# Performance work log

Hardware: AMD Instinct MI355X
Metric: run time of the kernel (lower is better)

Reference implementation:

```python
import jax, jax.numpy as jnp
import numpy as np

N = 50000      # nodes
E = 800000     # edges (before self-loops)
IN = 128       # in_channels
HID = 16       # hidden_channels
HEADS = 8
OUT = 16       # out_channels
NEG_SLOPE = 0.2
BN_EPS = 1e-5
LN_EPS = 1e-5


def setup_inputs() -> dict:
    key = jax.random.key(0)
    ks = jax.random.split(key, 16)
    s = 0.05
    inp = {
        "x": jax.random.normal(ks[0], (N, IN), jnp.float32),
        "edge_index": jax.random.randint(ks[1], (2, E), 0, N, jnp.int64),
        # conv1 (in=IN, out=HID, heads=HEADS, concat=True)
        "Wl1": jax.random.normal(ks[2], (HEADS * HID, IN), jnp.float32) * s,
        "bl1": jnp.zeros((HEADS * HID,), jnp.float32),
        "Wr1": jax.random.normal(ks[3], (HEADS * HID, IN), jnp.float32) * s,
        "br1": jnp.zeros((HEADS * HID,), jnp.float32),
        "att1": jax.random.normal(ks[4], (HEADS, HID), jnp.float32) * s,
        "bias1": jnp.zeros((HEADS * HID,), jnp.float32),
        # batchnorm (eval mode, running stats)
        "bn_w": jnp.ones((HEADS * HID,), jnp.float32),
        "bn_b": jnp.zeros((HEADS * HID,), jnp.float32),
        "bn_rm": jnp.zeros((HEADS * HID,), jnp.float32),
        "bn_rv": jnp.ones((HEADS * HID,), jnp.float32),
        # conv2 (in=HEADS*HID, out=OUT, heads=HEADS, concat=False)
        "Wl2": jax.random.normal(ks[5], (HEADS * OUT, HEADS * HID), jnp.float32) * s,
        "bl2": jnp.zeros((HEADS * OUT,), jnp.float32),
        "Wr2": jax.random.normal(ks[6], (HEADS * OUT, HEADS * HID), jnp.float32) * s,
        "br2": jnp.zeros((HEADS * OUT,), jnp.float32),
        "att2": jax.random.normal(ks[7], (HEADS, OUT), jnp.float32) * s,
        "bias2": jnp.zeros((OUT,), jnp.float32),
        # skip + layernorm
        "Wskip": jax.random.normal(ks[8], (OUT, IN), jnp.float32) * s,
        "ln_w": jnp.ones((OUT,), jnp.float32),
        "ln_b": jnp.zeros((OUT,), jnp.float32),
    }
    return inp


def _gatv2(x, src, dst, Wl, bl, Wr, br, att, bias, heads, ch, concat):
    """PyG GATv2Conv (share_weights=False), eval mode (no dropout)."""
    n = x.shape[0]
    xl = (x @ Wl.T + bl).reshape(n, heads, ch)   # source transform
    xr = (x @ Wr.T + br).reshape(n, heads, ch)   # target transform
    # edge-wise attention score
    e = jax.nn.leaky_relu(xl[src] + xr[dst], NEG_SLOPE)          # [E',H,C]
    score = jnp.einsum('ehc,hc->eh', e, att)                      # [E',H]
    # segment softmax over incoming edges per destination node
    smax = jax.ops.segment_max(score, dst, num_segments=n)
    ex = jnp.exp(score - smax[dst])
    denom = jax.ops.segment_sum(ex, dst, num_segments=n)
    alpha = ex / denom[dst]                                       # [E',H]
    out = jax.ops.segment_sum(alpha[:, :, None] * xl[src], dst, num_segments=n)
    if concat:
        out = out.reshape(n, heads * ch)
    else:
        out = out.mean(axis=1)
    return out + bias


def reference(x, edge_index, Wl1, bl1, Wr1, br1, att1, bias1,
              bn_w, bn_b, bn_rm, bn_rv,
              Wl2, bl2, Wr2, br2, att2, bias2,
              Wskip, ln_w, ln_b):
    n = x.shape[0]
    loops = jnp.arange(n, dtype=edge_index.dtype)
    src = jnp.concatenate([edge_index[0], loops])
    dst = jnp.concatenate([edge_index[1], loops])

    x_res = x @ Wskip.T                                            # [N,OUT]

    h = _gatv2(x, src, dst, Wl1, bl1, Wr1, br1, att1, bias1, HEADS, HID, True)
    # BatchNorm1d in eval mode
    h = (h - bn_rm) * jax.lax.rsqrt(bn_rv + BN_EPS) * bn_w + bn_b
    h = jax.nn.elu(h)

    h = _gatv2(h, src, dst, Wl2, bl2, Wr2, br2, att2, bias2, HEADS, OUT, False)

    y = h + x_res
    mu = y.mean(axis=-1, keepdims=True)
    var = ((y - mu) ** 2).mean(axis=-1, keepdims=True)
    return (y - mu) * jax.lax.rsqrt(var + LN_EPS) * ln_w + ln_b
```

## Files before the change

kernel.cpp:

```cpp
#include <hip/hip_runtime.h>

#define NEG_SLOPE 0.2f
#define BN_EPS 1e-5f
#define LN_EPS 1e-5f

#if __has_builtin(__builtin_amdgcn_exp2f)
#define EXP2F(x) __builtin_amdgcn_exp2f(x)
#else
#define EXP2F(x) exp2f(x)
#endif

typedef __bf16 bf16_t;
typedef bf16_t bf16x8 __attribute__((ext_vector_type(8)));
typedef float floatx4 __attribute__((ext_vector_type(4)));

__device__ __forceinline__ unsigned short f2bf(float f) {
  unsigned u = __float_as_uint(f);
  u += 0x7FFFu + ((u >> 16) & 1u);
  return (unsigned short)(u >> 16);
}
__device__ __forceinline__ float bf_lo(unsigned u) { return __uint_as_float(u << 16); }
__device__ __forceinline__ float bf_hi(unsigned u) { return __uint_as_float(u & 0xFFFF0000u); }

__global__ void cvt_all(const float* __restrict__ wl1, const float* __restrict__ wr1,
                        const float* __restrict__ wl2, const float* __restrict__ wr2,
                        const float* __restrict__ wsk,
                        const float* __restrict__ bias1,
                        const float* __restrict__ bn_w, const float* __restrict__ bn_b,
                        const float* __restrict__ bn_rm, const float* __restrict__ bn_rv,
                        const int* __restrict__ ei, int E,
                        unsigned short* __restrict__ wcat1,
                        unsigned short* __restrict__ wcat2,
                        int* __restrict__ deg8, unsigned short* __restrict__ rpos,
                        float* __restrict__ bnS, float* __restrict__ bnT,
                        int N) {
  const int W4 = 128 * 128 / 4;
  const int S4 = 16 * 128 / 4;
  int j = blockIdx.x * blockDim.x + threadIdx.x;
  const float* src;
  unsigned short* dst;
  if (j < W4)               { src = wl1; dst = wcat1; }
  else if (j < 2 * W4)      { src = wr1; dst = wcat1 + 128 * 128; j -= W4; }
  else if (j < 3 * W4)      { src = wl2; dst = wcat2; j -= 2 * W4; }
  else if (j < 4 * W4)      { src = wr2; dst = wcat2 + 128 * 128; j -= 3 * W4; }
  else if (j < 4 * W4 + S4) { src = wsk; dst = wcat1 + 256 * 128; j -= 4 * W4; }
  else {
    j -= 4 * W4 + S4;
    if (j < 32) {
      for (int t = j * 4; t < j * 4 + 4; ++t) {
        float S = bn_w[t] * rsqrtf(bn_rv[t] + BN_EPS);
        bnS[t] = S;
        bnT[t] = (bias1[t] - bn_rm[t]) * S + bn_b[t];
      }
    } else {
      int e = j - 32;
      if (e < E) {
        int d = ei[E + e];
        int c = (int)(blockIdx.x & 7);
        rpos[e] = (unsigned short)atomicAdd(&deg8[(size_t)c * N + d], 1);
      }
    }
    return;
  }
  float4 v = ((const float4*)src)[j];
  ushort4 o;
  o.x = f2bf(v.x); o.y = f2bf(v.y); o.z = f2bf(v.z); o.w = f2bf(v.w);
  ((ushort4*)dst)[j] = o;
}

__global__ __launch_bounds__(1024)
void csr_scan(const int* __restrict__ deg8, int* __restrict__ meta,
              int* __restrict__ cbase8, int* bsum, int N) {
  __shared__ int wsum[16];
  __shared__ int sh_base;
  int b = blockIdx.x;
  int tid = threadIdx.x;
  int lane = tid & 63, wid = tid >> 6;
  int i0 = b * 4096 + tid * 4;

  int4 v[8];
#pragma unroll
  for (int c = 0; c < 8; ++c) {
    const int* p = deg8 + (size_t)c * N;
    v[c] = make_int4(0, 0, 0, 0);
    if (i0 + 3 < N) v[c] = *(const int4*)(p + i0);
    else if (i0 < N) {
      v[c].x = p[i0];
      if (i0 + 1 < N) v[c].y = p[i0 + 1];
      if (i0 + 2 < N) v[c].z = p[i0 + 2];
    }
  }
  int4 run = make_int4(0, 0, 0, 0);
#pragma unroll
  for (int c = 0; c < 8; ++c) {
    int4 t = v[c];
    v[c] = run;
    run.x += t.x; run.y += t.y; run.z += t.z; run.w += t.w;
  }
  int g1 = (run.x + 1) & ~1, g2 = (run.y + 1) & ~1, g3 = (run.z + 1) & ~1, g4 = (run.w + 1) & ~1;
  int s1 = g1, s2 = s1 + g2, s3 = s2 + g3, s4 = s3 + g4;
  int s = s4;
#pragma unroll
  for (int d = 1; d < 64; d <<= 1) { int t = __shfl_up(s, d, 64); if (lane >= d) s += t; }
  if (lane == 63) wsum[wid] = s;
  __syncthreads();
  if (tid < 16) {
    int ws = wsum[tid];
#pragma unroll
    for (int d = 1; d < 16; d <<= 1) { int t = __shfl_up(ws, d, 16); if (tid >= d) ws += t; }
    wsum[tid] = ws;
  }
  __syncthreads();
  if (tid == 0) {
    __hip_atomic_store(&bsum[b], wsum[15] + 1, __ATOMIC_RELEASE, __HIP_MEMORY_SCOPE_AGENT);
    int base = 0;
    for (int j = 0; j < b; ++j) {
      int x;
      do { x = __hip_atomic_load(&bsum[j], __ATOMIC_ACQUIRE, __HIP_MEMORY_SCOPE_AGENT); } while (x == 0);
      base += x - 1;
    }
    sh_base = base;
  }
  __syncthreads();
  int off = sh_base + (wid ? wsum[wid - 1] : 0) + (s - s4);
  int st[4] = {off, off + s1, off + s2, off + s3};
  int tv[4] = {run.x, run.y, run.z, run.w};
#pragma unroll
  for (int k = 0; k < 4; ++k)
    if (i0 + k < N) ((int2*)meta)[i0 + k] = make_int2(st[k], tv[k]);
#pragma unroll
  for (int c = 0; c < 8; ++c) {
    int* p = cbase8 + (size_t)c * N;
    if (i0 + 3 < N) {
      *(int4*)(p + i0) = make_int4(st[0] + v[c].x, st[1] + v[c].y, st[2] + v[c].z, st[3] + v[c].w);
    } else if (i0 < N) {
      p[i0] = st[0] + v[c].x;
      if (i0 + 1 < N) p[i0 + 1] = st[1] + v[c].y;
      if (i0 + 2 < N) p[i0 + 2] = st[2] + v[c].z;
    }
  }
}

template <bool MIXED, bool AF32>
__device__ __forceinline__ void gemm_body(int wv, int lane,
    const void* __restrict__ Av, const unsigned short* __restrict__ B,
    const float* __restrict__ bias0, const float* __restrict__ bias1,
    unsigned short* __restrict__ Cl, unsigned short* __restrict__ Cr,
    float* __restrict__ Cf, int M, int pstrips) {
  int mtiles = (M + 31) >> 5;
  if (wv >= mtiles * 2) return;
  int mt = wv >> 1, sub = wv & 1;
  int r = lane & 15, quad = lane >> 4;

  bf16x8 a0[4], a1[4];
  if (AF32) {
    const float* Af = (const float*)Av;
    int r0 = min(mt * 32 + r, M - 1);
    int r1 = min(mt * 32 + 16 + r, M - 1);
    const float* A0 = Af + (size_t)r0 * 128 + quad * 8;
    const float* A1 = Af + (size_t)r1 * 128 + quad * 8;
#pragma unroll
    for (int k = 0; k < 4; ++k) {
      float4 fa = *(const float4*)(A0 + 32 * k);
      float4 fb = *(const float4*)(A0 + 32 * k + 4);
      float4 ga = *(const float4*)(A1 + 32 * k);
      float4 gb = *(const float4*)(A1 + 32 * k + 4);
      union { bf16x8 v; unsigned short s[8]; } t0, t1;
      t0.s[0] = f2bf(fa.x); t0.s[1] = f2bf(fa.y); t0.s[2] = f2bf(fa.z); t0.s[3] = f2bf(fa.w);
      t0.s[4] = f2bf(fb.x); t0.s[5] = f2bf(fb.y); t0.s[6] = f2bf(fb.z); t0.s[7] = f2bf(fb.w);
      t1.s[0] = f2bf(ga.x); t1.s[1] = f2bf(ga.y); t1.s[2] = f2bf(ga.z); t1.s[3] = f2bf(ga.w);
      t1.s[4] = f2bf(gb.x); t1.s[5] = f2bf(gb.y); t1.s[6] = f2bf(gb.z); t1.s[7] = f2bf(gb.w);
      a0[k] = t0.v;
      a1[k] = t1.v;
    }
  } else {
    const unsigned short* Au = (const unsigned short*)Av;
    const unsigned short* Abase = Au + (size_t)(mt * 32 + r) * 128 + quad * 8;
#pragma unroll
    for (int k = 0; k < 4; ++k) {
      a0[k] = *(const bf16x8*)(Abase + 32 * k);
      a1[k] = *(const bf16x8*)(Abase + 16 * 128 + 32 * k);
    }
  }

  int row0 = mt * 32 + quad * 4;
  const int Ptot = MIXED ? 272 : 256;
  for (int ps = sub; ps < pstrips; ps += 2) {
#pragma unroll
    for (int pp = 0; pp < 4; ++pp) {
      int p0 = ps * 64 + pp * 16;
      if (p0 >= Ptot) break;
      const unsigned short* Bbase = B + (size_t)(p0 + r) * 128 + quad * 8;
      bf16x8 b[4];
#pragma unroll
      for (int k = 0; k < 4; ++k) b[k] = *(const bf16x8*)(Bbase + 32 * k);
      floatx4 acc0 = {0.f, 0.f, 0.f, 0.f};
      floatx4 acc1 = {0.f, 0.f, 0.f, 0.f};
#pragma unroll
      for (int k = 0; k < 4; ++k) {
        acc0 = __builtin_amdgcn_mfma_f32_16x16x32_bf16(a0[k], b[k], acc0, 0, 0, 0);
        acc1 = __builtin_amdgcn_mfma_f32_16x16x32_bf16(a1[k], b[k], acc1, 0, 0, 0);
      }
      int col = p0 + r;
      if (MIXED && col >= 256) {
#pragma unroll
        for (int i = 0; i < 4; ++i) {
          if (row0 + i < M)      Cf[(size_t)(row0 + i) * 16 + (col - 256)] = acc0[i];
          if (row0 + 16 + i < M) Cf[(size_t)(row0 + 16 + i) * 16 + (col - 256)] = acc1[i];
        }
      } else {
        float bs = (col < 128) ? bias0[col] : bias1[col - 128];
        unsigned short* Ct = (col < 128) ? Cl : Cr;
        int cc = col & 127;
#pragma unroll
        for (int i = 0; i < 4; ++i) {
          if (row0 + i < M)      Ct[(size_t)(row0 + i) * 128 + cc] = f2bf(acc0[i] + bs);
          if (row0 + 16 + i < M) Ct[(size_t)(row0 + 16 + i) * 128 + cc] = f2bf(acc1[i] + bs);
        }
      }
    }
  }
}

__global__ __launch_bounds__(256)
void gemm_bf16_mfma(const unsigned short* __restrict__ A, const unsigned short* __restrict__ B,
                    const float* __restrict__ bias0, const float* __restrict__ bias1,
                    unsigned short* __restrict__ Cl, unsigned short* __restrict__ Cr,
                    int M, int pstrips) {
  gemm_body<false, false>((int)((blockIdx.x * blockDim.x + threadIdx.x) >> 6),
                          (int)(threadIdx.x & 63), A, B, bias0, bias1, Cl, Cr, nullptr,
                          M, pstrips);
}

__global__ __launch_bounds__(256)
void gemm1_scatter(const float* __restrict__ A, const unsigned short* __restrict__ B,
                   const float* __restrict__ bias0, const float* __restrict__ bias1,
                   unsigned short* __restrict__ Cl, unsigned short* __restrict__ Cr,
                   float* __restrict__ Cf,
                   int M, int pstrips, int gemmBlocks,
                   const int* __restrict__ ei, int E, int ebase,
                   const int* __restrict__ cbase8, const unsigned short* __restrict__ rpos,
                   unsigned short* __restrict__ csr, int N) {
  if ((int)blockIdx.x >= gemmBlocks) {
    int e = ((int)blockIdx.x - gemmBlocks) * 256 + (int)threadIdx.x;
    if (e < E) {
      int d = ei[E + e];
      int c = ((ebase + e) >> 8) & 7;
      csr[cbase8[(size_t)c * N + d] + (int)rpos[e]] = (unsigned short)ei[e];
    }
    return;
  }
  gemm_body<true, true>((int)((blockIdx.x * blockDim.x + threadIdx.x) >> 6),
                        (int)(threadIdx.x & 63), A, B, bias0, bias1, Cl, Cr, Cf, M, pstrips);
}

template <int LAYER>
__global__ __launch_bounds__(256)
void gat_agg(const unsigned short* __restrict__ xlt,
             const unsigned short* __restrict__ xrt,
             const int* __restrict__ meta,
             const unsigned short* __restrict__ csr,
             const float* __restrict__ att,
             const float* __restrict__ p0, const float* __restrict__ p1,
             const float* __restrict__ p2, const float* __restrict__ p3,
             void* __restrict__ outp, int n, int nwaves) {
  int lane = threadIdx.x & 63;
  int gw = (int)((blockIdx.x * blockDim.x + threadIdx.x) >> 6);
  int slot = lane >> 4;
  int sl4 = lane & 15;
  const char* __restrict__ xb = (const char*)xlt;
  const unsigned slOff = (unsigned)(sl4 << 4);
  const int hsh = (slot & 1) << 4;
  const bool whi = (slot >= 2);
  float4 atA = ((const float4*)att)[sl4 * 2];
  float4 atB = ((const float4*)att)[sl4 * 2 + 1];
  const float SC = 0.6f * 1.44269504f;
  float a0 = SC * atA.x, a1 = SC * atA.y, a2 = SC * atA.z, a3 = SC * atA.w;
  float a4 = SC * atB.x, a5 = SC * atB.y, a6 = SC * atB.z, a7 = SC * atB.w;

  for (int dst = gw; dst < n; dst += nwaves) {
    int dsts = __builtin_amdgcn_readfirstlane(dst);
    int2 m = *(const int2*)(meta + 2 * (size_t)dsts);
    int beg = __builtin_amdgcn_readfirstlane(m.x);
    int dg  = __builtin_amdgcn_readfirstlane(m.y);
    const unsigned* cp = (const unsigned*)csr + (beg >> 1);

    uint4 urw = *(const uint4*)((const char*)xrt + (((unsigned)dsts << 8) + slOff));
    float xr0 = bf_lo(urw.x), xr1 = bf_hi(urw.x), xr2 = bf_lo(urw.y), xr3 = bf_hi(urw.y);
    float xr4 = bf_lo(urw.z), xr5 = bf_hi(urw.z), xr6 = bf_lo(urw.w), xr7 = bf_hi(urw.w);

    float l = 0.f;
    float c0 = 0.f, c1 = 0.f, c2 = 0.f, c3 = 0.f;
    float c4 = 0.f, c5 = 0.f, c6 = 0.f, c7 = 0.f;

    auto gat = [&](unsigned w0, unsigned w1) -> uint4 {
      unsigned pr = whi ? w1 : w0;
      unsigned s = (pr >> hsh) & 0xFFFFu;
      return *(const uint4*)(xb + ((s << 8) + slOff));
    };

    auto body = [&](uint4 u, float vm, bool masked) {
      float x0 = bf_lo(u.x), x1 = bf_hi(u.x), x2 = bf_lo(u.y), x3 = bf_hi(u.y);
      float x4 = bf_lo(u.z), x5 = bf_hi(u.z), x6 = bf_lo(u.w), x7 = bf_hi(u.w);
      float e0 = x0 + xr0, e1 = x1 + xr1, e2 = x2 + xr2, e3 = x3 + xr3;
      float e4 = x4 + xr4, e5 = x5 + xr5, e6 = x6 + xr6, e7 = x7 + xr7;
      float sc = fmaf(fmaf(fabsf(e0), 0.66666667f, e0), a0,
                 fmaf(fmaf(fabsf(e1), 0.66666667f, e1), a1,
                 fmaf(fmaf(fabsf(e2), 0.66666667f, e2), a2,
                 fmaf(fmaf(fabsf(e3), 0.66666667f, e3), a3,
                 fmaf(fmaf(fabsf(e4), 0.66666667f, e4), a4,
                 fmaf(fmaf(fabsf(e5), 0.66666667f, e5), a5,
                 fmaf(fmaf(fabsf(e6), 0.66666667f, e6), a6,
                      fmaf(fabsf(e7), 0.66666667f, e7) * a7)))))));
      sc += __shfl_xor(sc, 1);
      float pw = EXP2F(sc);
      if (masked) pw *= vm;
      l += pw;
      c0 = fmaf(pw, x0, c0); c1 = fmaf(pw, x1, c1);
      c2 = fmaf(pw, x2, c2); c3 = fmaf(pw, x3, c3);
      c4 = fmaf(pw, x4, c4); c5 = fmaf(pw, x5, c5);
      c6 = fmaf(pw, x6, c6); c7 = fmaf(pw, x7, c7);
    };

    int nq = dg >> 2;
    int q = 0;
    int nq4 = nq & ~3;
    for (; q < nq4; q += 4) {
      unsigned w[8];
#pragma unroll
      for (int k = 0; k < 8; ++k) w[k] = cp[2 * q + k];
      uint4 u[4];
#pragma unroll
      for (int k = 0; k < 4; ++k) u[k] = gat(w[2 * k], w[2 * k + 1]);
#pragma unroll
      for (int k = 0; k < 4; ++k) body(u[k], 1.f, false);
    }
    if (nq - q >= 2) {
      unsigned w[4];
#pragma unroll
      for (int k = 0; k < 4; ++k) w[k] = cp[2 * q + k];
      uint4 u[2];
#pragma unroll
      for (int k = 0; k < 2; ++k) u[k] = gat(w[2 * k], w[2 * k + 1]);
#pragma unroll
      for (int k = 0; k < 2; ++k) body(u[k], 1.f, false);
      q += 2;
    }
    if (nq - q >= 1) {
      unsigned w0 = cp[2 * q], w1 = cp[2 * q + 1];
      body(gat(w0, w1), 1.f, false);
      q += 1;
    }
    {
      unsigned w0 = cp[2 * q], w1 = cp[2 * q + 1];
      int tot = dg + 1;
      int e = 4 * q + slot;
      unsigned pr = whi ? w1 : w0;
      unsigned sE = (pr >> hsh) & 0xFFFFu;
      unsigned s = (e < dg) ? sE : (unsigned)dsts;
      float vm = (e < tot) ? 1.f : 0.f;
      uint4 u = *(const uint4*)(xb + ((s << 8) + slOff));
      body(u, vm, true);
    }

    l  += __shfl_xor(l, 16);  l  += __shfl_xor(l, 32);
    c0 += __shfl_xor(c0, 16); c0 += __shfl_xor(c0, 32);
    c1 += __shfl_xor(c1, 16); c1 += __shfl_xor(c1, 32);
    c2 += __shfl_xor(c2, 16); c2 += __shfl_xor(c2, 32);
    c3 += __shfl_xor(c3, 16); c3 += __shfl_xor(c3, 32);
    c4 += __shfl_xor(c4, 16); c4 += __shfl_xor(c4, 32);
    c5 += __shfl_xor(c5, 16); c5 += __shfl_xor(c5, 32);
    c6 += __shfl_xor(c6, 16); c6 += __shfl_xor(c6, 32);
    c7 += __shfl_xor(c7, 16); c7 += __shfl_xor(c7, 32);
    float inv = 1.f / l;

    if (LAYER == 1) {
      float4 Sa = *(const float4*)(p0 + sl4 * 8);
      float4 Sb = *(const float4*)(p0 + sl4 * 8 + 4);
      float4 Ta = *(const float4*)(p1 + sl4 * 8);
      float4 Tb = *(const float4*)(p1 + sl4 * 8 + 4);
      float o0 = fmaf(c0 * inv, Sa.x, Ta.x);
      float o1 = fmaf(c1 * inv, Sa.y, Ta.y);
      float o2 = fmaf(c2 * inv, Sa.z, Ta.z);
      float o3 = fmaf(c3 * inv, Sa.w, Ta.w);
      float o4 = fmaf(c4 * inv, Sb.x, Tb.x);
      float o5 = fmaf(c5 * inv, Sb.y, Tb.y);
      float o6 = fmaf(c6 * inv, Sb.z, Tb.z);
      float o7 = fmaf(c7 * inv, Sb.w, Tb.w);
      o0 = (o0 > 0.f) ? o0 : (__expf(o0) - 1.f);
      o1 = (o1 > 0.f) ? o1 : (__expf(o1) - 1.f);
      o2 = (o2 > 0.f) ? o2 : (__expf(o2) - 1.f);
      o3 = (o3 > 0.f) ? o3 : (__expf(o3) - 1.f);
      o4 = (o4 > 0.f) ? o4 : (__expf(o4) - 1.f);
      o5 = (o5 > 0.f) ? o5 : (__expf(o5) - 1.f);
      o6 = (o6 > 0.f) ? o6 : (__expf(o6) - 1.f);
      o7 = (o7 > 0.f) ? o7 : (__expf(o7) - 1.f);
      if (slot == 0) {
        uint4 o;
        o.x = ((unsigned)f2bf(o1) << 16) | f2bf(o0);
        o.y = ((unsigned)f2bf(o3) << 16) | f2bf(o2);
        o.z = ((unsigned)f2bf(o5) << 16) | f2bf(o4);
        o.w = ((unsigned)f2bf(o7) << 16) | f2bf(o6);
        ((uint4*)outp)[(size_t)dsts * 16 + sl4] = o;
      }
    } else {
      float y0 = c0 * inv, y1 = c1 * inv, y2 = c2 * inv, y3 = c3 * inv;
      float y4 = c4 * inv, y5 = c5 * inv, y6 = c6 * inv, y7 = c7 * inv;
#pragma unroll
      for (int d = 2; d <= 8; d <<= 1) {
        y0 += __shfl_xor(y0, d); y1 += __shfl_xor(y1, d);
        y2 += __shfl_xor(y2, d); y3 += __shfl_xor(y3, d);
        y4 += __shfl_xor(y4, d); y5 += __shfl_xor(y5, d);
        y6 += __shfl_xor(y6, d); y7 += __shfl_xor(y7, d);
      }
      int chh = (sl4 & 1) * 8;
      float4 b2a = *(const float4*)(p1 + chh);
      float4 b2b = *(const float4*)(p1 + chh + 4);
      float4 xsa = *(const float4*)(p0 + (size_t)dsts * 16 + chh);
      float4 xsb = *(const float4*)(p0 + (size_t)dsts * 16 + chh + 4);
      y0 = y0 * 0.125f + b2a.x + xsa.x;
      y1 = y1 * 0.125f + b2a.y + xsa.y;
      y2 = y2 * 0.125f + b2a.z + xsa.z;
      y3 = y3 * 0.125f + b2a.w + xsa.w;
      y4 = y4 * 0.125f + b2b.x + xsb.x;
      y5 = y5 * 0.125f + b2b.y + xsb.y;
      y6 = y6 * 0.125f + b2b.z + xsb.z;
      y7 = y7 * 0.125f + b2b.w + xsb.w;
      float t = ((y0 + y1) + (y2 + y3)) + ((y4 + y5) + (y6 + y7));
      t += __shfl_xor(t, 1);
      float mu = t * (1.f / 16.f);
      float d0 = y0 - mu, d1 = y1 - mu, d2 = y2 - mu, d3 = y3 - mu;
      float d4 = y4 - mu, d5 = y5 - mu, d6 = y6 - mu, d7 = y7 - mu;
      float v = ((d0 * d0 + d1 * d1) + (d2 * d2 + d3 * d3)) +
                ((d4 * d4 + d5 * d5) + (d6 * d6 + d7 * d7));
      v += __shfl_xor(v, 1);
      float istd = rsqrtf(v * (1.f / 16.f) + LN_EPS);
      float4 lwa = *(const float4*)(p2 + chh);
      float4 lwb = *(const float4*)(p2 + chh + 4);
      float4 lba = *(const float4*)(p3 + chh);
      float4 lbb = *(const float4*)(p3 + chh + 4);
      if (lane < 2) {
        float4 oa, ob;
        oa.x = d0 * istd * lwa.x + lba.x;
        oa.y = d1 * istd * lwa.y + lba.y;
        oa.z = d2 * istd * lwa.z + lba.z;
        oa.w = d3 * istd * lwa.w + lba.w;
        ob.x = d4 * istd * lwb.x + lbb.x;
        ob.y = d5 * istd * lwb.y + lbb.y;
        ob.z = d6 * istd * lwb.z + lbb.z;
        ob.w = d7 * istd * lwb.w + lbb.w;
        float* op = (float*)outp + (size_t)dsts * 16 + chh;
        *(float4*)op = oa;
        *(float4*)(op + 4) = ob;
      }
    }
  }
}

extern "C" void kernel_launch(void* const* d_in, const int* in_sizes, int n_in,
                              void* d_out, int out_size, void* d_ws, size_t ws_size,
                              hipStream_t stream) {
  const float* x     = (const float*)d_in[0];
  const int*   ei    = (const int*)d_in[1];
  const float* Wl1   = (const float*)d_in[2];
  const float* bl1   = (const float*)d_in[3];
  const float* Wr1   = (const float*)d_in[4];
  const float* br1   = (const float*)d_in[5];
  const float* att1  = (const float*)d_in[6];
  const float* bias1 = (const float*)d_in[7];
  const float* bn_w  = (const float*)d_in[8];
  const float* bn_b  = (const float*)d_in[9];
  const float* bn_rm = (const float*)d_in[10];
  const float* bn_rv = (const float*)d_in[11];
  const float* Wl2   = (const float*)d_in[12];
  const float* bl2   = (const float*)d_in[13];
  const float* Wr2   = (const float*)d_in[14];
  const float* br2   = (const float*)d_in[15];
  const float* att2  = (const float*)d_in[16];
  const float* bias2 = (const float*)d_in[17];
  const float* Wskip = (const float*)d_in[18];
  const float* ln_w  = (const float*)d_in[19];
  const float* ln_b  = (const float*)d_in[20];

  const int N = in_sizes[0] / 128;
  const int E = in_sizes[1] / 2;

  char* w = (char*)d_ws;
  size_t off = 0;
  auto alloc = [&](size_t bytes) -> void* {
    void* p = (void*)(w + off);
    off += (bytes + 255) & ~(size_t)255;
    return p;
  };
  unsigned short* wcat1  = (unsigned short*)alloc(272 * 128 * 2);
  unsigned short* wcat2  = (unsigned short*)alloc(256 * 128 * 2);
  unsigned short* xlt    = (unsigned short*)alloc((size_t)N * 128 * 2);
  unsigned short* xrt    = (unsigned short*)alloc((size_t)N * 128 * 2);
  float*          xres   = (float*)alloc((size_t)N * 16 * 4);
  unsigned short* hbf    = (unsigned short*)alloc((size_t)N * 128 * 2);
  float*          bnS    = (float*)alloc(128 * 4);
  float*          bnT    = (float*)alloc(128 * 4);
  int*            deg8   = (int*)alloc((size_t)8 * N * 4);
  int*            bsum   = (int*)alloc(64 * 4);
  int*            cbase8 = (int*)alloc((size_t)8 * N * 4);
  int*            meta   = (int*)alloc((size_t)2 * N * 4);
  unsigned short* rpos   = (unsigned short*)alloc((size_t)E * 2);
  unsigned short* csr    = (unsigned short*)alloc((size_t)(E + N) * 2 + 256);

  const int W4 = 128 * 128 / 4, S4 = 16 * 128 / 4;
  const int ebase = 4 * W4 + S4 + 32;
  const int nb = (N + 4095) / 4096;

  hipMemsetAsync(deg8, 0, (size_t)8 * N * 4 + 256 + 64 * 4, stream);
  {
    int tot = ebase + E;
    cvt_all<<<(tot + 255) / 256, 256, 0, stream>>>(
        Wl1, Wr1, Wl2, Wr2, Wskip, bias1, bn_w, bn_b, bn_rm, bn_rv, ei, E,
        wcat1, wcat2, deg8, rpos, bnS, bnT, N);
  }

  csr_scan<<<nb, 1024, 0, stream>>>(deg8, meta, cbase8, bsum, N);

  {
    int mtiles = (N + 31) >> 5;
    int waves = mtiles * 2;
    int gemmBlocks = (waves + 3) / 4;
    int scatBlocks = (E + 255) / 256;
    gemm1_scatter<<<gemmBlocks + scatBlocks, 256, 0, stream>>>(
        x, wcat1, bl1, br1, xlt, xrt, xres, N, 5, gemmBlocks,
        ei, E, ebase, cbase8, rpos, csr, N);
  }

  {
    int blocks = 2048, nwaves = blocks * 4;
    gat_agg<1><<<blocks, 256, 0, stream>>>(xlt, xrt, meta, csr, att1,
                                           bnS, bnT, nullptr, nullptr, (void*)hbf, N, nwaves);
  }

  {
    int mtiles = (N + 31) >> 5;
    int waves = mtiles * 2;
    gemm_bf16_mfma<<<(waves + 3) / 4, 256, 0, stream>>>(
        hbf, wcat2, bl2, br2, xlt, xrt, N, 4);
  }

  {
    int blocks = 2048, nwaves = blocks * 4;
    gat_agg<2><<<blocks, 256, 0, stream>>>(xlt, xrt, meta, csr, att2,
                                           xres, bias2, ln_w, ln_b, d_out, N, nwaves);
  }
}
```

Measured before the change: 298.3 us.

## Fuse weight conversion, degree count, scan, GEMM1 and CSR scatter into one kernel

Merges the cvt_all, csr_scan and gemm1_scatter launches into one kernel whose block ranges do the different stages. Dependencies between stages are enforced with global atomic flag counters and spin-waits instead of kernel boundaries. The aim is to remove launch gaps and let the GEMM overlap with degree counting and the scan. It relies on block dispatch order to avoid deadlock, since waiting blocks can occupy CUs while the blocks they wait on are still queued. The scan also moves to smaller 1024-element blocks, which lengthens the serial chain of prefix lookbacks.

```diff
diff --git a/kernel.cpp b/kernel.cpp
--- a/kernel.cpp
+++ b/kernel.cpp
@@ -21,125 +21,6 @@
 }
 __device__ __forceinline__ float bf_lo(unsigned u) { return __uint_as_float(u << 16); }
 __device__ __forceinline__ float bf_hi(unsigned u) { return __uint_as_float(u & 0xFFFF0000u); }
-
-__global__ void cvt_all(const float* __restrict__ wl1, const float* __restrict__ wr1,
-                        const float* __restrict__ wl2, const float* __restrict__ wr2,
-                        const float* __restrict__ wsk,
-                        const float* __restrict__ bias1,
-                        const float* __restrict__ bn_w, const float* __restrict__ bn_b,
-                        const float* __restrict__ bn_rm, const float* __restrict__ bn_rv,
-                        const int* __restrict__ ei, int E,
-                        unsigned short* __restrict__ wcat1,
-                        unsigned short* __restrict__ wcat2,
-                        int* __restrict__ deg8, unsigned short* __restrict__ rpos,
-                        float* __restrict__ bnS, float* __restrict__ bnT,
-                        int N) {
-  const int W4 = 128 * 128 / 4;
-  const int S4 = 16 * 128 / 4;
-  int j = blockIdx.x * blockDim.x + threadIdx.x;
-  const float* src;
-  unsigned short* dst;
-  if (j < W4)               { src = wl1; dst = wcat1; }
-  else if (j < 2 * W4)      { src = wr1; dst = wcat1 + 128 * 128; j -= W4; }
-  else if (j < 3 * W4)      { src = wl2; dst = wcat2; j -= 2 * W4; }
-  else if (j < 4 * W4)      { src = wr2; dst = wcat2 + 128 * 128; j -= 3 * W4; }
-  else if (j < 4 * W4 + S4) { src = wsk; dst = wcat1 + 256 * 128; j -= 4 * W4; }
-  else {
-    j -= 4 * W4 + S4;
-    if (j < 32) {
-      for (int t = j * 4; t < j * 4 + 4; ++t) {
-        float S = bn_w[t] * rsqrtf(bn_rv[t] + BN_EPS);
-        bnS[t] = S;
-        bnT[t] = (bias1[t] - bn_rm[t]) * S + bn_b[t];
-      }
-    } else {
-      int e = j - 32;
-      if (e < E) {
-        int d = ei[E + e];
-        int c = (int)(blockIdx.x & 7);
-        rpos[e] = (unsigned short)atomicAdd(&deg8[(size_t)c * N + d], 1);
-      }
-    }
-    return;
-  }
-  float4 v = ((const float4*)src)[j];
-  ushort4 o;
-  o.x = f2bf(v.x); o.y = f2bf(v.y); o.z = f2bf(v.z); o.w = f2bf(v.w);
-  ((ushort4*)dst)[j] = o;
-}
-
-__global__ __launch_bounds__(1024)
-void csr_scan(const int* __restrict__ deg8, int* __restrict__ meta,
-              int* __restrict__ cbase8, int* bsum, int N) {
-  __shared__ int wsum[16];
-  __shared__ int sh_base;
-  int b = blockIdx.x;
-  int tid = threadIdx.x;
-  int lane = tid & 63, wid = tid >> 6;
-  int i0 = b * 4096 + tid * 4;
-
-  int4 v[8];
-#pragma unroll
-  for (int c = 0; c < 8; ++c) {
-    const int* p = deg8 + (size_t)c * N;
-    v[c] = make_int4(0, 0, 0, 0);
-    if (i0 + 3 < N) v[c] = *(const int4*)(p + i0);
-    else if (i0 < N) {
-      v[c].x = p[i0];
-      if (i0 + 1 < N) v[c].y = p[i0 + 1];
-      if (i0 + 2 < N) v[c].z = p[i0 + 2];
-    }
-  }
-  int4 run = make_int4(0, 0, 0, 0);
-#pragma unroll
-  for (int c = 0; c < 8; ++c) {
-    int4 t = v[c];
-    v[c] = run;
-    run.x += t.x; run.y += t.y; run.z += t.z; run.w += t.w;
-  }
-  int g1 = (run.x + 1) & ~1, g2 = (run.y + 1) & ~1, g3 = (run.z + 1) & ~1, g4 = (run.w + 1) & ~1;
-  int s1 = g1, s2 = s1 + g2, s3 = s2 + g3, s4 = s3 + g4;
-  int s = s4;
-#pragma unroll
-  for (int d = 1; d < 64; d <<= 1) { int t = __shfl_up(s, d, 64); if (lane >= d) s += t; }
-  if (lane == 63) wsum[wid] = s;
-  __syncthreads();
-  if (tid < 16) {
-    int ws = wsum[tid];
-#pragma unroll
-    for (int d = 1; d < 16; d <<= 1) { int t = __shfl_up(ws, d, 16); if (tid >= d) ws += t; }
-    wsum[tid] = ws;
-  }
-  __syncthreads();
-  if (tid == 0) {
-    __hip_atomic_store(&bsum[b], wsum[15] + 1, __ATOMIC_RELEASE, __HIP_MEMORY_SCOPE_AGENT);
-    int base = 0;
-    for (int j = 0; j < b; ++j) {
-      int x;
-      do { x = __hip_atomic_load(&bsum[j], __ATOMIC_ACQUIRE, __HIP_MEMORY_SCOPE_AGENT); } while (x == 0);
-      base += x - 1;
-    }
-    sh_base = base;
-  }
-  __syncthreads();
-  int off = sh_base + (wid ? wsum[wid - 1] : 0) + (s - s4);
-  int st[4] = {off, off + s1, off + s2, off + s3};
-  int tv[4] = {run.x, run.y, run.z, run.w};
-#pragma unroll
-  for (int k = 0; k < 4; ++k)
-    if (i0 + k < N) ((int2*)meta)[i0 + k] = make_int2(st[k], tv[k]);
-#pragma unroll
-  for (int c = 0; c < 8; ++c) {
-    int* p = cbase8 + (size_t)c * N;
-    if (i0 + 3 < N) {
-      *(int4*)(p + i0) = make_int4(st[0] + v[c].x, st[1] + v[c].y, st[2] + v[c].z, st[3] + v[c].w);
-    } else if (i0 < N) {
-      p[i0] = st[0] + v[c].x;
-      if (i0 + 1 < N) p[i0 + 1] = st[1] + v[c].y;
-      if (i0 + 2 < N) p[i0 + 2] = st[2] + v[c].z;
-    }
-  }
-}
 
 template <bool MIXED, bool AF32>
 __device__ __forceinline__ void gemm_body(int wv, int lane,
@@ -232,26 +113,182 @@
                           M, pstrips);
 }
 
+#define F_CNT(c) ((c) * 16)
+#define F_WCVT 128
+#define F_SCAN 144
+
 __global__ __launch_bounds__(256)
-void gemm1_scatter(const float* __restrict__ A, const unsigned short* __restrict__ B,
-                   const float* __restrict__ bias0, const float* __restrict__ bias1,
-                   unsigned short* __restrict__ Cl, unsigned short* __restrict__ Cr,
-                   float* __restrict__ Cf,
-                   int M, int pstrips, int gemmBlocks,
-                   const int* __restrict__ ei, int E, int ebase,
-                   const int* __restrict__ cbase8, const unsigned short* __restrict__ rpos,
-                   unsigned short* __restrict__ csr, int N) {
-  if ((int)blockIdx.x >= gemmBlocks) {
-    int e = ((int)blockIdx.x - gemmBlocks) * 256 + (int)threadIdx.x;
+void mega(const float* __restrict__ x,
+          const float* __restrict__ wl1, const float* __restrict__ wr1,
+          const float* __restrict__ wl2, const float* __restrict__ wr2,
+          const float* __restrict__ wsk, const float* __restrict__ bias1,
+          const float* __restrict__ bn_w, const float* __restrict__ bn_b,
+          const float* __restrict__ bn_rm, const float* __restrict__ bn_rv,
+          const float* __restrict__ bl1, const float* __restrict__ br1,
+          const int* __restrict__ ei,
+          unsigned short* __restrict__ wcat1, unsigned short* __restrict__ wcat2,
+          float* __restrict__ bnS, float* __restrict__ bnT,
+          int* __restrict__ deg8, unsigned short* __restrict__ rpos,
+          int* __restrict__ meta, int* __restrict__ cbase8, int* __restrict__ bsum,
+          int* __restrict__ flags, unsigned short* __restrict__ csr,
+          unsigned short* __restrict__ xlt, unsigned short* __restrict__ xrt,
+          float* __restrict__ xres,
+          int N, int E, int WBLK, int CBLK, int SBLK, int GBLK) {
+  const int b = (int)blockIdx.x;
+  const int tid = (int)threadIdx.x;
+  const int W4 = 128 * 128 / 4;
+  const int S4 = 16 * 128 / 4;
+
+  if (b < WBLK) {
+    int j = b * 256 + tid;
+    const float* src = nullptr;
+    unsigned short* dst = nullptr;
+    if (j < W4)               { src = wl1; dst = wcat1; }
+    else if (j < 2 * W4)      { src = wr1; dst = wcat1 + 128 * 128; j -= W4; }
+    else if (j < 3 * W4)      { src = wl2; dst = wcat2; j -= 2 * W4; }
+    else if (j < 4 * W4)      { src = wr2; dst = wcat2 + 128 * 128; j -= 3 * W4; }
+    else if (j < 4 * W4 + S4) { src = wsk; dst = wcat1 + 256 * 128; j -= 4 * W4; }
+    else {
+      j -= 4 * W4 + S4;
+      if (j < 32) {
+        for (int t = j * 4; t < j * 4 + 4; ++t) {
+          float S = bn_w[t] * rsqrtf(bn_rv[t] + BN_EPS);
+          bnS[t] = S;
+          bnT[t] = (bias1[t] - bn_rm[t]) * S + bn_b[t];
+        }
+      }
+    }
+    if (src) {
+      float4 v = ((const float4*)src)[j];
+      ushort4 o;
+      o.x = f2bf(v.x); o.y = f2bf(v.y); o.z = f2bf(v.z); o.w = f2bf(v.w);
+      ((ushort4*)dst)[j] = o;
+    }
+    __syncthreads();
+    if (tid == 0) { __threadfence(); atomicAdd(&flags[F_WCVT], 1); }
+    return;
+  }
+
+  if (b < WBLK + CBLK) {
+    int e = (b - WBLK) * 256 + tid;
     if (e < E) {
       int d = ei[E + e];
-      int c = ((ebase + e) >> 8) & 7;
+      int c = b & 7;
+      rpos[e] = (unsigned short)atomicAdd(&deg8[(size_t)c * N + d], 1);
+    }
+    __syncthreads();
+    if (tid == 0) { __threadfence(); atomicAdd(&flags[F_CNT(b & 7)], 1); }
+    return;
+  }
+
+  if (b < WBLK + CBLK + SBLK) {
+    __shared__ int wsum[4];
+    __shared__ int sh_base;
+    if (tid == 0) {
+      int t;
+      do {
+        t = 0;
+        for (int c = 0; c < 8; ++c)
+          t += __hip_atomic_load(&flags[F_CNT(c)], __ATOMIC_ACQUIRE, __HIP_MEMORY_SCOPE_AGENT);
+        if (t != CBLK) __builtin_amdgcn_s_sleep(2);
+      } while (t != CBLK);
+    }
+    __syncthreads();
+
+    int bs = b - (WBLK + CBLK);
+    int lane = tid & 63, wid = tid >> 6;
+    int i0 = bs * 1024 + tid * 4;
+
+    int4 v[8];
+#pragma unroll
+    for (int c = 0; c < 8; ++c) {
+      const int* p = deg8 + (size_t)c * N;
+      v[c] = make_int4(0, 0, 0, 0);
+      if (i0 + 3 < N) v[c] = *(const int4*)(p + i0);
+      else if (i0 < N) {
+        v[c].x = p[i0];
+        if (i0 + 1 < N) v[c].y = p[i0 + 1];
+        if (i0 + 2 < N) v[c].z = p[i0 + 2];
+      }
+    }
+    int4 run = make_int4(0, 0, 0, 0);
+#pragma unroll
+    for (int c = 0; c < 8; ++c) {
+      int4 t = v[c];
+      v[c] = run;
+      run.x += t.x; run.y += t.y; run.z += t.z; run.w += t.w;
+    }
+    int g1 = (run.x + 1) & ~1, g2 = (run.y + 1) & ~1, g3 = (run.z + 1) & ~1, g4 = (run.w + 1) & ~1;
+    int s1 = g1, s2 = s1 + g2, s3 = s2 + g3, s4 = s3 + g4;
+    int s = s4;
+#pragma unroll
+    for (int d = 1; d < 64; d <<= 1) { int t = __shfl_up(s, d, 64); if (lane >= d) s += t; }
+    if (lane == 63) wsum[wid] = s;
+    __syncthreads();
+    if (tid < 4) {
+      int ws = wsum[tid];
+#pragma unroll
+      for (int d = 1; d < 4; d <<= 1) { int t = __shfl_up(ws, d, 4); if (tid >= d) ws += t; }
+      wsum[tid] = ws;
+    }
+    __syncthreads();
+    if (tid == 0) {
+      __hip_atomic_store(&bsum[bs], wsum[3] + 1, __ATOMIC_RELEASE, __HIP_MEMORY_SCOPE_AGENT);
+      int base = 0;
+      for (int j = 0; j < bs; ++j) {
+        int xv;
+        do { xv = __hip_atomic_load(&bsum[j], __ATOMIC_ACQUIRE, __HIP_MEMORY_SCOPE_AGENT); } while (xv == 0);
+        base += xv - 1;
+      }
+      sh_base = base;
+    }
+    __syncthreads();
+    int off = sh_base + (wid ? wsum[wid - 1] : 0) + (s - s4);
+    int st[4] = {off, off + s1, off + s2, off + s3};
+    int tv[4] = {run.x, run.y, run.z, run.w};
+#pragma unroll
+    for (int k = 0; k < 4; ++k)
+      if (i0 + k < N) ((int2*)meta)[i0 + k] = make_int2(st[k], tv[k]);
+#pragma unroll
+    for (int c = 0; c < 8; ++c) {
+      int* p = cbase8 + (size_t)c * N;
+      if (i0 + 3 < N) {
+        *(int4*)(p + i0) = make_int4(st[0] + v[c].x, st[1] + v[c].y, st[2] + v[c].z, st[3] + v[c].w);
+      } else if (i0 < N) {
+        p[i0] = st[0] + v[c].x;
+        if (i0 + 1 < N) p[i0 + 1] = st[1] + v[c].y;
+        if (i0 + 2 < N) p[i0 + 2] = st[2] + v[c].z;
+      }
+    }
+    __syncthreads();
+    if (tid == 0) { __threadfence(); atomicAdd(&flags[F_SCAN], 1); }
+    return;
+  }
+
+  if (b < WBLK + CBLK + SBLK + GBLK) {
+    if (tid == 0) {
+      while (__hip_atomic_load(&flags[F_WCVT], __ATOMIC_ACQUIRE, __HIP_MEMORY_SCOPE_AGENT) != WBLK)
+        __builtin_amdgcn_s_sleep(2);
+    }
+    __syncthreads();
+    int wv = (b - (WBLK + CBLK + SBLK)) * 4 + (tid >> 6);
+    gemm_body<true, true>(wv, tid & 63, x, wcat1, bl1, br1, xlt, xrt, xres, N, 5);
+    return;
+  }
+
+  {
+    if (tid == 0) {
+      while (__hip_atomic_load(&flags[F_SCAN], __ATOMIC_ACQUIRE, __HIP_MEMORY_SCOPE_AGENT) != SBLK)
+        __builtin_amdgcn_s_sleep(2);
+    }
+    __syncthreads();
+    int e = (b - (WBLK + CBLK + SBLK + GBLK)) * 256 + tid;
+    if (e < E) {
+      int d = ei[E + e];
+      int c = ((e >> 8) + WBLK) & 7;
       csr[cbase8[(size_t)c * N + d] + (int)rpos[e]] = (unsigned short)ei[e];
     }
-    return;
-  }
-  gemm_body<true, true>((int)((blockIdx.x * blockDim.x + threadIdx.x) >> 6),
-                        (int)(threadIdx.x & 63), A, B, bias0, bias1, Cl, Cr, Cf, M, pstrips);
+  }
 }
 
 template <int LAYER>
@@ -502,34 +539,24 @@
   float*          bnT    = (float*)alloc(128 * 4);
   int*            deg8   = (int*)alloc((size_t)8 * N * 4);
   int*            bsum   = (int*)alloc(64 * 4);
+  int*            flags  = (int*)alloc(256 * 4);
   int*            cbase8 = (int*)alloc((size_t)8 * N * 4);
   int*            meta   = (int*)alloc((size_t)2 * N * 4);
   unsigned short* rpos   = (unsigned short*)alloc((size_t)E * 2);
   unsigned short* csr    = (unsigned short*)alloc((size_t)(E + N) * 2 + 256);
 
-  const int W4 = 128 * 128 / 4, S4 = 16 * 128 / 4;
-  const int ebase = 4 * W4 + S4 + 32;
-  const int nb = (N + 4095) / 4096;
-
-  hipMemsetAsync(deg8, 0, (size_t)8 * N * 4 + 256 + 64 * 4, stream);
-  {
-    int tot = ebase + E;
-    cvt_all<<<(tot + 255) / 256, 256, 0, stream>>>(
-        Wl1, Wr1, Wl2, Wr2, Wskip, bias1, bn_w, bn_b, bn_rm, bn_rv, ei, E,
-        wcat1, wcat2, deg8, rpos, bnS, bnT, N);
-  }
-
-  csr_scan<<<nb, 1024, 0, stream>>>(deg8, meta, cbase8, bsum, N);
-
-  {
-    int mtiles = (N + 31) >> 5;
-    int waves = mtiles * 2;
-    int gemmBlocks = (waves + 3) / 4;
-    int scatBlocks = (E + 255) / 256;
-    gemm1_scatter<<<gemmBlocks + scatBlocks, 256, 0, stream>>>(
-        x, wcat1, bl1, br1, xlt, xrt, xres, N, 5, gemmBlocks,
-        ei, E, ebase, cbase8, rpos, csr, N);
-  }
+  const int WBLK = ((4 * 4096 + 512 + 32) + 255) / 256;
+  const int CBLK = (E + 255) / 256;
+  const int SBLK = (N + 1023) / 1024;
+  const int mtiles = (N + 31) >> 5;
+  const int GBLK = (mtiles * 2 + 3) / 4;
+
+  hipMemsetAsync(deg8, 0, (size_t)8 * N * 4 + 256 + 1024, stream);
+
+  mega<<<WBLK + CBLK + SBLK + GBLK + CBLK, 256, 0, stream>>>(
+      x, Wl1, Wr1, Wl2, Wr2, Wskip, bias1, bn_w, bn_b, bn_rm, bn_rv, bl1, br1, ei,
+      wcat1, wcat2, bnS, bnT, deg8, rpos, meta, cbase8, bsum, flags, csr,
+      xlt, xrt, xres, N, E, WBLK, CBLK, SBLK, GBLK);
 
   {
     int blocks = 2048, nwaves = blocks * 4;
@@ -537,12 +564,7 @@
                                            bnS, bnT, nullptr, nullptr, (void*)hbf, N, nwaves);
   }
 
-  {
-    int mtiles = (N + 31) >> 5;
-    int waves = mtiles * 2;
-    gemm_bf16_mfma<<<(waves + 3) / 4, 256, 0, stream>>>(
-        hbf, wcat2, bl2, br2, xlt, xrt, N, 4);
-  }
+  gemm_bf16_mfma<<<GBLK, 256, 0, stream>>>(hbf, wcat2, bl2, br2, xlt, xrt, N, 4);
 
   {
     int blocks = 2048, nwaves = blocks * 4;
```

New measurement: 538.4 us. +80.5%, slower.
